# Kernel tuning notes

Measured on AMD Instinct MI355X. Metric: run time of the kernel, lower is better.

The kernel has to match this reference:

```python
import jax, jax.numpy as jnp
import numpy as np

N = 100000
E = 1600000
IN_DIM = 128
H = 8
D = 16


def setup_inputs() -> dict:
    key = jax.random.key(0)
    ks = jax.random.split(key, 9)
    h = jax.random.normal(ks[0], (N, IN_DIM), dtype=jnp.float32)
    src = jax.random.randint(ks[1], (E,), 0, N, dtype=jnp.int32)
    dst = jax.random.randint(ks[2], (E,), 0, N, dtype=jnp.int32)
    s = 1.0 / np.sqrt(IN_DIM)
    WQ = jax.random.normal(ks[3], (IN_DIM, H * D), dtype=jnp.float32) * s
    WK = jax.random.normal(ks[4], (IN_DIM, H * D), dtype=jnp.float32) * s
    WV = jax.random.normal(ks[5], (IN_DIM, H * D), dtype=jnp.float32) * s
    bQ = jax.random.normal(ks[6], (H * D,), dtype=jnp.float32) * 0.01
    bK = jax.random.normal(ks[7], (H * D,), dtype=jnp.float32) * 0.01
    bV = jax.random.normal(ks[8], (H * D,), dtype=jnp.float32) * 0.01
    return {"h": h, "WQ": WQ, "bQ": bQ, "WK": WK, "bK": bK, "WV": WV, "bV": bV,
            "src": src, "dst": dst}


def reference(h, WQ, bQ, WK, bK, WV, bV, src, dst):
    # Node projections -> [N, H, D]
    Q = (h @ WQ + bQ).reshape(-1, H, D)
    K = (h @ WK + bK).reshape(-1, H, D)
    V = (h @ WV + bV).reshape(-1, H, D)
    scale = jnp.float32(np.sqrt(D))
    # Edge-wise score: src-dot-dst per head, clamped exp. [E, H]
    score = jnp.exp(jnp.clip(jnp.sum(K[src] * Q[dst], axis=-1) / scale, -5.0, 5.0))
    # Scatter-sum aggregation to destination nodes.
    wV = jax.ops.segment_sum(score[:, :, None] * V[src], dst, num_segments=N)  # [N,H,D]
    z = jax.ops.segment_sum(score, dst, num_segments=N)  # [N,H]
    return wV / z[:, :, None]
```

## Files before the change

kernel.cpp:

```cpp
#include <hip/hip_runtime.h>

#define HD 128

typedef float f4v __attribute__((ext_vector_type(4)));
typedef float f32x4 __attribute__((ext_vector_type(4)));
typedef short short8 __attribute__((ext_vector_type(8)));
typedef _Float16 h8 __attribute__((ext_vector_type(8)));

__device__ inline void bf16split(float f, unsigned short& hi, unsigned short& lo) {
    unsigned u = __builtin_bit_cast(unsigned, f);
    unsigned short h = (unsigned short)((u + 0x7FFFu + ((u >> 16) & 1u)) >> 16);
    float fh = __builtin_bit_cast(float, (unsigned)h << 16);
    float r = f - fh;
    unsigned v = __builtin_bit_cast(unsigned, r);
    unsigned short l = (unsigned short)((v + 0x7FFFu + ((v >> 16) & 1u)) >> 16);
    hi = h; lo = l;
}

__global__ __launch_bounds__(256) void prep_kernel(
    const float* __restrict__ WQ, const float* __restrict__ WK,
    const float* __restrict__ WV,
    const float* __restrict__ bQ, const float* __restrict__ bK,
    const float* __restrict__ bV,
    unsigned short* __restrict__ Whi, unsigned short* __restrict__ Wlo,
    float* __restrict__ bcat)
{
    const int blk = blockIdx.x, tid = threadIdx.x;
    if (blk == 96) {
        for (int j = tid; j < 384; j += 256) {
            const float* b = (j < 128) ? bQ : (j < 256) ? bK : bV;
            bcat[j] = b[j & 127];
        }
        return;
    }
    const int kt = blk / 24, nf = blk % 24;
    #pragma unroll
    for (int t = 0; t < 2; ++t) {
        int idx = t * 256 + tid;
        int l = idx >> 3, e = idx & 7;
        int k = kt * 32 + ((l >> 4) << 3) + e;
        int j = nf * 16 + (l & 15);
        const float* W = (j < 128) ? WQ : (j < 256) ? WK : WV;
        float f = W[(size_t)k * 128 + (j & 127)];
        unsigned short hi, lo;
        bf16split(f, hi, lo);
        Whi[(size_t)blk * 512 + idx] = hi;
        Wlo[(size_t)blk * 512 + idx] = lo;
    }
}

__global__ __launch_bounds__(512, 2) void qkv_kernel(
    const float* __restrict__ h,
    const unsigned short* __restrict__ Whi, const unsigned short* __restrict__ Wlo,
    const float* __restrict__ bcat,
    float* __restrict__ Q, _Float16* __restrict__ KV, int N)
{
    __shared__ unsigned short hsh[64 * 136];
    __shared__ unsigned short hsl[64 * 136];
    const int tid = threadIdx.x;
    const int r0 = blockIdx.x * 64;

    #pragma unroll
    for (int jj = 0; jj < 4; ++jj) {
        int idf4 = jj * 512 + tid;
        int row = idf4 >> 5;
        int c4 = (idf4 & 31) << 2;
        f4v v = {0.f, 0.f, 0.f, 0.f};
        if (r0 + row < N)
            v = __builtin_nontemporal_load((const f4v*)(h + (size_t)(r0 + row) * 128 + c4));
        ushort4 hv, lv;
        bf16split(v[0], hv.x, lv.x);
        bf16split(v[1], hv.y, lv.y);
        bf16split(v[2], hv.z, lv.z);
        bf16split(v[3], hv.w, lv.w);
        *(ushort4*)&hsh[row * 136 + c4] = hv;
        *(ushort4*)&hsl[row * 136 + c4] = lv;
    }
    __syncthreads();

    const int wid = tid >> 6, l = tid & 63;
    const int lrow = l & 15;
    const int lkOff = (l >> 4) << 3;

    f32x4 acc[4][3];
    #pragma unroll
    for (int mf = 0; mf < 4; ++mf)
        #pragma unroll
        for (int n3 = 0; n3 < 3; ++n3)
            acc[mf][n3] = (f32x4){0.f, 0.f, 0.f, 0.f};

    #pragma unroll
    for (int kt = 0; kt < 4; ++kt) {
        short8 ah[4], al[4];
        #pragma unroll
        for (int mf = 0; mf < 4; ++mf) {
            int off = (mf * 16 + lrow) * 136 + kt * 32 + lkOff;
            ah[mf] = *(const short8*)&hsh[off];
            al[mf] = *(const short8*)&hsl[off];
        }
        short8 bh[3], bl[3];
        #pragma unroll
        for (int n3 = 0; n3 < 3; ++n3) {
            size_t fb = ((size_t)(kt * 24 + wid * 3 + n3)) * 512 + l * 8;
            bh[n3] = *(const short8*)&Whi[fb];
            bl[n3] = *(const short8*)&Wlo[fb];
        }
        #pragma unroll
        for (int mf = 0; mf < 4; ++mf)
            #pragma unroll
            for (int n3 = 0; n3 < 3; ++n3) {
                acc[mf][n3] = __builtin_amdgcn_mfma_f32_16x16x32_bf16(ah[mf], bh[n3], acc[mf][n3], 0, 0, 0);
                acc[mf][n3] = __builtin_amdgcn_mfma_f32_16x16x32_bf16(ah[mf], bl[n3], acc[mf][n3], 0, 0, 0);
                acc[mf][n3] = __builtin_amdgcn_mfma_f32_16x16x32_bf16(al[mf], bh[n3], acc[mf][n3], 0, 0, 0);
            }
    }

    #pragma unroll
    for (int n3 = 0; n3 < 3; ++n3) {
        int n0 = (wid * 3 + n3) * 16;
        int col = n0 + lrow;
        float bb = bcat[col];
        #pragma unroll
        for (int mf = 0; mf < 4; ++mf)
            #pragma unroll
            for (int r = 0; r < 4; ++r) {
                int grow = r0 + mf * 16 + ((l >> 4) << 2) + r;
                if (grow >= N) continue;
                float val = acc[mf][n3][r] + bb;
                if (col < 128) {
                    Q[(size_t)grow * HD + col] = val;
                } else if (col < 256) {
                    int j = col - 128;
                    KV[(size_t)grow * 256 + ((j >> 2) << 3) + (j & 3)] = (_Float16)val;
                } else {
                    int j = col - 256;
                    KV[(size_t)grow * 256 + ((j >> 2) << 3) + 4 + (j & 3)] = (_Float16)val;
                }
            }
    }
}

__global__ __launch_bounds__(256) void rank_kernel(
    const int* __restrict__ dst, int* __restrict__ U,
    int* __restrict__ rank, int E)
{
    int e = blockIdx.x * 256 + threadIdx.x;
    if (e < E) {
        int r = atomicAdd(&U[dst[e]], 1);
        __builtin_nontemporal_store(r, &rank[e]);
    }
}

__global__ __launch_bounds__(256) void scan_a(
    const int* __restrict__ C, int* __restrict__ tileSum, int N)
{
    __shared__ int red[256];
    const int t = blockIdx.x, tid = threadIdx.x;
    int base = t * 1024 + tid * 4;
    int s = 0;
    #pragma unroll
    for (int i = 0; i < 4; ++i)
        if (base + i < N) s += C[base + i];
    red[tid] = s;
    __syncthreads();
    for (int off = 128; off > 0; off >>= 1) {
        if (tid < off) red[tid] += red[tid + off];
        __syncthreads();
    }
    if (tid == 0) tileSum[t] = red[0];
}

__global__ __launch_bounds__(1024) void scan_b(
    const int* __restrict__ tileSum, int* __restrict__ tileOff, int numTiles)
{
    __shared__ int buf[1024];
    const int t = threadIdx.x;
    int v = (t < numTiles) ? tileSum[t] : 0;
    buf[t] = v;
    __syncthreads();
    for (int off = 1; off < 1024; off <<= 1) {
        int x = (t >= off) ? buf[t - off] : 0;
        __syncthreads();
        buf[t] += x;
        __syncthreads();
    }
    if (t < numTiles) tileOff[t] = buf[t] - v;
}

__global__ __launch_bounds__(256) void scan_c(
    const int* __restrict__ C, const int* __restrict__ tileOff,
    int* __restrict__ O, int N, int E)
{
    __shared__ int buf[256];
    const int t = blockIdx.x, tid = threadIdx.x;
    int base = t * 1024 + tid * 4;
    int c[4];
    #pragma unroll
    for (int i = 0; i < 4; ++i)
        c[i] = (base + i < N) ? C[base + i] : 0;
    int tsum = c[0] + c[1] + c[2] + c[3];
    buf[tid] = tsum;
    __syncthreads();
    for (int off = 1; off < 256; off <<= 1) {
        int x = (tid >= off) ? buf[tid - off] : 0;
        __syncthreads();
        buf[tid] += x;
        __syncthreads();
    }
    int run = buf[tid] - tsum + tileOff[t];
    #pragma unroll
    for (int i = 0; i < 4; ++i) {
        if (base + i < N) O[base + i] = run;
        run += c[i];
    }
    if (t == 0 && tid == 0) O[N] = E;
}

__global__ __launch_bounds__(256) void scatter_kernel(
    const int* __restrict__ src, const int* __restrict__ dst,
    const int* __restrict__ O, const int* __restrict__ rank,
    int* __restrict__ srclist, int E)
{
    int e = blockIdx.x * 256 + threadIdx.x;
    if (e < E) {
        __builtin_nontemporal_store(src[e], &srclist[O[dst[e]] + rank[e]]);
    }
}

__global__ __launch_bounds__(256) void agg_kernel(
    const float* __restrict__ Q, const _Float16* __restrict__ KV,
    const int* __restrict__ O, const int* __restrict__ srclist,
    float* __restrict__ out, int N)
{
    const int l = threadIdx.x & 63;
    const int n = blockIdx.x * 4 + (threadIdx.x >> 6);
    if (n >= N) return;

    const int half = l >> 5;
    const int c = l & 31;
    const int c4 = c * 4;

    f4v q = __builtin_nontemporal_load((const f4v*)(Q + (size_t)n * HD + c4));
    f4v acc = {0.f, 0.f, 0.f, 0.f};
    float z = 0.f;
    const int start = __builtin_nontemporal_load(&O[n]);
    const int end   = __builtin_nontemporal_load(&O[n + 1]);

    for (int base = start; base < end; base += 64) {
        int sv = 0;
        if (base + l < end) sv = __builtin_nontemporal_load(&srclist[base + l]);
        const int cnt = min(64, end - base);
        int j = 0;
        for (; j + 16 <= cnt; j += 16) {
            h8 kv[8];
            #pragma unroll
            for (int u = 0; u < 8; ++u) {
                int s = __shfl(sv, j + 2 * u + half);
                kv[u] = *(const h8*)(KV + (size_t)s * 256 + c * 8);
            }
            #pragma unroll
            for (int u = 0; u < 8; ++u) {
                float p = fmaf((float)kv[u][0], q[0],
                          fmaf((float)kv[u][1], q[1],
                          fmaf((float)kv[u][2], q[2], (float)kv[u][3] * q[3])));
                p += __shfl_xor(p, 1);
                p += __shfl_xor(p, 2);
                float sc = __expf(fminf(5.f, fmaxf(-5.f, p * 0.25f)));
                z += sc;
                acc[0] = fmaf(sc, (float)kv[u][4], acc[0]);
                acc[1] = fmaf(sc, (float)kv[u][5], acc[1]);
                acc[2] = fmaf(sc, (float)kv[u][6], acc[2]);
                acc[3] = fmaf(sc, (float)kv[u][7], acc[3]);
            }
        }
        for (; j + 8 <= cnt; j += 8) {
            h8 kv[4];
            #pragma unroll
            for (int u = 0; u < 4; ++u) {
                int s = __shfl(sv, j + 2 * u + half);
                kv[u] = *(const h8*)(KV + (size_t)s * 256 + c * 8);
            }
            #pragma unroll
            for (int u = 0; u < 4; ++u) {
                float p = fmaf((float)kv[u][0], q[0],
                          fmaf((float)kv[u][1], q[1],
                          fmaf((float)kv[u][2], q[2], (float)kv[u][3] * q[3])));
                p += __shfl_xor(p, 1);
                p += __shfl_xor(p, 2);
                float sc = __expf(fminf(5.f, fmaxf(-5.f, p * 0.25f)));
                z += sc;
                acc[0] = fmaf(sc, (float)kv[u][4], acc[0]);
                acc[1] = fmaf(sc, (float)kv[u][5], acc[1]);
                acc[2] = fmaf(sc, (float)kv[u][6], acc[2]);
                acc[3] = fmaf(sc, (float)kv[u][7], acc[3]);
            }
        }
        for (; j < cnt; j += 2) {
            int e = j + half;
            bool valid = e < cnt;
            int s = __shfl(sv, valid ? e : j);
            h8 kv = *(const h8*)(KV + (size_t)s * 256 + c * 8);
            float p = fmaf((float)kv[0], q[0],
                      fmaf((float)kv[1], q[1],
                      fmaf((float)kv[2], q[2], (float)kv[3] * q[3])));
            p += __shfl_xor(p, 1);
            p += __shfl_xor(p, 2);
            float sc = __expf(fminf(5.f, fmaxf(-5.f, p * 0.25f)));
            if (!valid) sc = 0.f;
            z += sc;
            acc[0] = fmaf(sc, (float)kv[4], acc[0]);
            acc[1] = fmaf(sc, (float)kv[5], acc[1]);
            acc[2] = fmaf(sc, (float)kv[6], acc[2]);
            acc[3] = fmaf(sc, (float)kv[7], acc[3]);
        }
    }

    acc[0] += __shfl_xor(acc[0], 32);
    acc[1] += __shfl_xor(acc[1], 32);
    acc[2] += __shfl_xor(acc[2], 32);
    acc[3] += __shfl_xor(acc[3], 32);
    z      += __shfl_xor(z, 32);

    if (half == 0) {
        f4v res = acc / z;
        __builtin_nontemporal_store(res, (f4v*)(out + (size_t)n * HD + c4));
    }
}

extern "C" void kernel_launch(void* const* d_in, const int* in_sizes, int n_in,
                              void* d_out, int out_size, void* d_ws, size_t ws_size,
                              hipStream_t stream)
{
    const float* h  = (const float*)d_in[0];
    const float* WQ = (const float*)d_in[1];
    const float* bQ = (const float*)d_in[2];
    const float* WK = (const float*)d_in[3];
    const float* bK = (const float*)d_in[4];
    const float* WV = (const float*)d_in[5];
    const float* bV = (const float*)d_in[6];
    const int* src  = (const int*)d_in[7];
    const int* dst  = (const int*)d_in[8];
    float* out = (float*)d_out;

    const int N = in_sizes[0] / 128;
    const int E = in_sizes[7];
    const int numTiles = (N + 1023) / 1024;

    char* w = (char*)d_ws;
    auto alloc = [&](size_t bytes) {
        char* p = w;
        w += (bytes + 255) & ~(size_t)255;
        return p;
    };
    float* Q      = (float*)alloc((size_t)N * HD * 4);
    _Float16* KV  = (_Float16*)alloc((size_t)N * 256 * 2);
    int* O        = (int*)alloc((size_t)(N + 1) * 4);
    int* U        = (int*)alloc((size_t)N * 4);
    int* rank     = (int*)alloc((size_t)E * 4);
    int* tileSum  = (int*)alloc((size_t)numTiles * 4);
    int* tileOff  = (int*)alloc((size_t)numTiles * 4);
    int* srclist  = (int*)alloc((size_t)E * 4);
    unsigned short* Whi = (unsigned short*)alloc((size_t)96 * 512 * 2);
    unsigned short* Wlo = (unsigned short*)alloc((size_t)96 * 512 * 2);
    float* bcat   = (float*)alloc(384 * 4);

    hipMemsetAsync(U, 0, (size_t)N * 4, stream);

    prep_kernel<<<97, 256, 0, stream>>>(WQ, WK, WV, bQ, bK, bV, Whi, Wlo, bcat);
    qkv_kernel<<<(N + 63) / 64, 512, 0, stream>>>(h, Whi, Wlo, bcat, Q, KV, N);
    rank_kernel<<<(E + 255) / 256, 256, 0, stream>>>(dst, U, rank, E);
    scan_a<<<numTiles, 256, 0, stream>>>(U, tileSum, N);
    scan_b<<<1, 1024, 0, stream>>>(tileSum, tileOff, numTiles);
    scan_c<<<numTiles, 256, 0, stream>>>(U, tileOff, O, N, E);
    scatter_kernel<<<(E + 255) / 256, 256, 0, stream>>>(src, dst, O, rank, srclist, E);
    agg_kernel<<<(N + 3) / 4, 256, 0, stream>>>(Q, KV, O, srclist, out, N);
}
```

Baseline: 410.9 us.

## Replace per-node atomic CSR build with two-level bucketed counting sort

Replaces the global per-edge atomic rank, three-pass scan and random scatter with a two-level counting sort. Edges are first histogrammed into 512-node buckets, bucket-scattered through LDS-staged chunks into an intermediate buffer, then each bucket builds its local CSR offsets and source list in shared memory. This is meant to cut global atomic contention and the random 4-byte writes to srclist, at the cost of an extra 8-byte-per-edge intermediate buffer and more kernel passes. It assumes NBk is at most 256 buckets, and edge order within a node becomes nondeterministic.

```diff
diff --git a/kernel.cpp b/kernel.cpp
--- a/kernel.cpp
+++ b/kernel.cpp
@@ -140,90 +140,141 @@
     }
 }
 
-__global__ __launch_bounds__(256) void rank_kernel(
-    const int* __restrict__ dst, int* __restrict__ U,
-    int* __restrict__ rank, int E)
-{
-    int e = blockIdx.x * 256 + threadIdx.x;
-    if (e < E) {
-        int r = atomicAdd(&U[dst[e]], 1);
-        __builtin_nontemporal_store(r, &rank[e]);
-    }
-}
-
-__global__ __launch_bounds__(256) void scan_a(
-    const int* __restrict__ C, int* __restrict__ tileSum, int N)
-{
-    __shared__ int red[256];
-    const int t = blockIdx.x, tid = threadIdx.x;
-    int base = t * 1024 + tid * 4;
-    int s = 0;
-    #pragma unroll
-    for (int i = 0; i < 4; ++i)
-        if (base + i < N) s += C[base + i];
-    red[tid] = s;
-    __syncthreads();
-    for (int off = 128; off > 0; off >>= 1) {
-        if (tid < off) red[tid] += red[tid + off];
-        __syncthreads();
-    }
-    if (tid == 0) tileSum[t] = red[0];
-}
-
-__global__ __launch_bounds__(1024) void scan_b(
-    const int* __restrict__ tileSum, int* __restrict__ tileOff, int numTiles)
-{
-    __shared__ int buf[1024];
+
+__global__ __launch_bounds__(256) void bhist_kernel(
+    const int* __restrict__ dst, int* __restrict__ bucketCnt, int E, int NBk)
+{
+    __shared__ int hst[512];
+    for (int i = threadIdx.x; i < NBk; i += 256) hst[i] = 0;
+    __syncthreads();
+    for (int e = blockIdx.x * 256 + threadIdx.x; e < E; e += gridDim.x * 256)
+        atomicAdd(&hst[dst[e] >> 9], 1);
+    __syncthreads();
+    for (int i = threadIdx.x; i < NBk; i += 256)
+        if (hst[i]) atomicAdd(&bucketCnt[i], hst[i]);
+}
+
+__global__ __launch_bounds__(256) void bscan_kernel(
+    const int* __restrict__ bucketCnt, int* __restrict__ bucketBase,
+    int* __restrict__ bucketCursor, int NBk)
+{
+    __shared__ int sc[256];
     const int t = threadIdx.x;
-    int v = (t < numTiles) ? tileSum[t] : 0;
-    buf[t] = v;
-    __syncthreads();
-    for (int off = 1; off < 1024; off <<= 1) {
-        int x = (t >= off) ? buf[t - off] : 0;
-        __syncthreads();
-        buf[t] += x;
-        __syncthreads();
-    }
-    if (t < numTiles) tileOff[t] = buf[t] - v;
-}
-
-__global__ __launch_bounds__(256) void scan_c(
-    const int* __restrict__ C, const int* __restrict__ tileOff,
-    int* __restrict__ O, int N, int E)
-{
-    __shared__ int buf[256];
-    const int t = blockIdx.x, tid = threadIdx.x;
-    int base = t * 1024 + tid * 4;
-    int c[4];
-    #pragma unroll
-    for (int i = 0; i < 4; ++i)
-        c[i] = (base + i < N) ? C[base + i] : 0;
-    int tsum = c[0] + c[1] + c[2] + c[3];
-    buf[tid] = tsum;
+    int v = (t < NBk) ? bucketCnt[t] : 0;
+    sc[t] = v;
     __syncthreads();
     for (int off = 1; off < 256; off <<= 1) {
-        int x = (tid >= off) ? buf[tid - off] : 0;
-        __syncthreads();
-        buf[tid] += x;
-        __syncthreads();
-    }
-    int run = buf[tid] - tsum + tileOff[t];
-    #pragma unroll
-    for (int i = 0; i < 4; ++i) {
-        if (base + i < N) O[base + i] = run;
-        run += c[i];
-    }
-    if (t == 0 && tid == 0) O[N] = E;
-}
-
-__global__ __launch_bounds__(256) void scatter_kernel(
+        int x = (t >= off) ? sc[t - off] : 0;
+        __syncthreads();
+        sc[t] += x;
+        __syncthreads();
+    }
+    if (t < NBk) {
+        int base = sc[t] - v;
+        bucketBase[t] = base;
+        bucketCursor[t] = base;
+    }
+    if (t == NBk - 1) bucketBase[NBk] = sc[t];
+}
+
+#define SC_CHUNK 8192
+__global__ __launch_bounds__(1024, 1) void bscatter_kernel(
     const int* __restrict__ src, const int* __restrict__ dst,
-    const int* __restrict__ O, const int* __restrict__ rank,
-    int* __restrict__ srclist, int E)
-{
-    int e = blockIdx.x * 256 + threadIdx.x;
-    if (e < E) {
-        __builtin_nontemporal_store(src[e], &srclist[O[dst[e]] + rank[e]]);
+    int* __restrict__ bucketCursor, int2* __restrict__ ebuf, int E, int NBk)
+{
+    __shared__ int cnt[256], sc[256], lbase[256], lcur[256], gdst[256];
+    __shared__ int2 buf[SC_CHUNK];
+    __shared__ short bkt[SC_CHUNK];
+    const int tid = threadIdx.x;
+    const int e0 = blockIdx.x * SC_CHUNK;
+    const int count = min(SC_CHUNK, E - e0);
+
+    for (int i = tid; i < 256; i += 1024) cnt[i] = 0;
+    __syncthreads();
+
+    int d8[8], s8[8], b8[8];
+    #pragma unroll
+    for (int u = 0; u < 8; ++u) {
+        int i = u * 1024 + tid;
+        if (i < count) {
+            d8[u] = dst[e0 + i];
+            s8[u] = src[e0 + i];
+            b8[u] = d8[u] >> 9;
+            atomicAdd(&cnt[b8[u]], 1);
+        }
+    }
+    __syncthreads();
+
+    if (tid < 256) sc[tid] = cnt[tid];
+    __syncthreads();
+    for (int off = 1; off < 256; off <<= 1) {
+        int x = (tid < 256 && tid >= off) ? sc[tid - off] : 0;
+        __syncthreads();
+        if (tid < 256) sc[tid] += x;
+        __syncthreads();
+    }
+    if (tid < 256) {
+        lbase[tid] = sc[tid] - cnt[tid];
+        lcur[tid] = lbase[tid];
+        if (tid < NBk && cnt[tid])
+            gdst[tid] = atomicAdd(&bucketCursor[tid], cnt[tid]);
+    }
+    __syncthreads();
+
+    #pragma unroll
+    for (int u = 0; u < 8; ++u) {
+        int i = u * 1024 + tid;
+        if (i < count) {
+            int p = atomicAdd(&lcur[b8[u]], 1);
+            buf[p] = make_int2(s8[u], d8[u]);
+            bkt[p] = (short)b8[u];
+        }
+    }
+    __syncthreads();
+
+    for (int i = tid; i < count; i += 1024) {
+        int b = bkt[i];
+        ebuf[gdst[b] + (i - lbase[b])] = buf[i];
+    }
+}
+
+__global__ __launch_bounds__(1024, 1) void bcsr_kernel(
+    const int2* __restrict__ ebuf, const int* __restrict__ bucketBase,
+    int* __restrict__ O, int* __restrict__ srclist, int N, int E, int NBk)
+{
+    __shared__ int hst[512], sc[512], pre[512], cur[512];
+    const int b = blockIdx.x, tid = threadIdx.x;
+    const int nodes0 = b << 9;
+    const int nn = min(512, N - nodes0);
+    const int e0 = bucketBase[b], e1 = bucketBase[b + 1];
+    const int cnt = e1 - e0;
+
+    for (int i = tid; i < 512; i += 1024) hst[i] = 0;
+    __syncthreads();
+    for (int i = tid; i < cnt; i += 1024)
+        atomicAdd(&hst[ebuf[e0 + i].y & 511], 1);
+    __syncthreads();
+
+    if (tid < 512) sc[tid] = hst[tid];
+    __syncthreads();
+    for (int off = 1; off < 512; off <<= 1) {
+        int x = (tid < 512 && tid >= off) ? sc[tid - off] : 0;
+        __syncthreads();
+        if (tid < 512) sc[tid] += x;
+        __syncthreads();
+    }
+    if (tid < 512) {
+        pre[tid] = sc[tid] - hst[tid];
+        cur[tid] = pre[tid];
+        if (tid < nn) O[nodes0 + tid] = e0 + pre[tid];
+    }
+    if (b == NBk - 1 && tid == 0) O[N] = E;
+    __syncthreads();
+
+    for (int i = tid; i < cnt; i += 1024) {
+        int2 p = ebuf[e0 + i];
+        int pos = atomicAdd(&cur[p.y & 511], 1);
+        srclist[e0 + pos] = p.x;
     }
 }
 
@@ -344,7 +395,7 @@
 
     const int N = in_sizes[0] / 128;
     const int E = in_sizes[7];
-    const int numTiles = (N + 1023) / 1024;
+    const int NBk = (N + 511) >> 9;
 
     char* w = (char*)d_ws;
     auto alloc = [&](size_t bytes) {
@@ -355,23 +406,23 @@
     float* Q      = (float*)alloc((size_t)N * HD * 4);
     _Float16* KV  = (_Float16*)alloc((size_t)N * 256 * 2);
     int* O        = (int*)alloc((size_t)(N + 1) * 4);
-    int* U        = (int*)alloc((size_t)N * 4);
-    int* rank     = (int*)alloc((size_t)E * 4);
-    int* tileSum  = (int*)alloc((size_t)numTiles * 4);
-    int* tileOff  = (int*)alloc((size_t)numTiles * 4);
+    int2* ebuf    = (int2*)alloc((size_t)E * 8);
     int* srclist  = (int*)alloc((size_t)E * 4);
+    int* bucketCnt    = (int*)alloc((size_t)(NBk + 1) * 4);
+    int* bucketBase   = (int*)alloc((size_t)(NBk + 1) * 4);
+    int* bucketCursor = (int*)alloc((size_t)(NBk + 1) * 4);
     unsigned short* Whi = (unsigned short*)alloc((size_t)96 * 512 * 2);
     unsigned short* Wlo = (unsigned short*)alloc((size_t)96 * 512 * 2);
     float* bcat   = (float*)alloc(384 * 4);
 
-    hipMemsetAsync(U, 0, (size_t)N * 4, stream);
+    hipMemsetAsync(bucketCnt, 0, (size_t)(NBk + 1) * 4, stream);
 
     prep_kernel<<<97, 256, 0, stream>>>(WQ, WK, WV, bQ, bK, bV, Whi, Wlo, bcat);
     qkv_kernel<<<(N + 63) / 64, 512, 0, stream>>>(h, Whi, Wlo, bcat, Q, KV, N);
-    rank_kernel<<<(E + 255) / 256, 256, 0, stream>>>(dst, U, rank, E);
-    scan_a<<<numTiles, 256, 0, stream>>>(U, tileSum, N);
-    scan_b<<<1, 1024, 0, stream>>>(tileSum, tileOff, numTiles);
-    scan_c<<<numTiles, 256, 0, stream>>>(U, tileOff, O, N, E);
-    scatter_kernel<<<(E + 255) / 256, 256, 0, stream>>>(src, dst, O, rank, srclist, E);
+    bhist_kernel<<<512, 256, 0, stream>>>(dst, bucketCnt, E, NBk);
+    bscan_kernel<<<1, 256, 0, stream>>>(bucketCnt, bucketBase, bucketCursor, NBk);
+    bscatter_kernel<<<(E + SC_CHUNK - 1) / SC_CHUNK, 1024, 0, stream>>>(
+        src, dst, bucketCursor, ebuf, E, NBk);
+    bcsr_kernel<<<NBk, 1024, 0, stream>>>(ebuf, bucketBase, O, srclist, N, E, NBk);
     agg_kernel<<<(N + 3) / 4, 256, 0, stream>>>(Q, KV, O, srclist, out, N);
 }
```

After: 333.1 us. 18.9% less time.
